# Performance work log

Measured on AMD Instinct MI355X. Metric: run time of the kernel, lower is better.

The kernel has to match this reference:

```python
import jax, jax.numpy as jnp
import numpy as np

N_NODES = 100000


def setup_inputs() -> dict:
    key = jax.random.key(0)
    k1, k2, k3, k4 = jax.random.split(key, 4)
    E = 1600000
    D_IN, D_OUT = 128, 128
    feat = jax.random.normal(k1, (N_NODES, D_IN), dtype=jnp.float32)
    src = jax.random.randint(k2, (E,), 0, N_NODES, dtype=jnp.int32)
    dst = jax.random.randint(k3, (E,), 0, N_NODES, dtype=jnp.int32)
    # xavier_uniform for weight [in, out]
    limit = float(np.sqrt(6.0 / (D_IN + D_OUT)))
    weight = jax.random.uniform(k4, (D_IN, D_OUT), dtype=jnp.float32,
                                minval=-limit, maxval=limit)
    bias = jnp.zeros((D_OUT,), dtype=jnp.float32)
    return {"feat": feat, "weight": weight, "bias": bias, "src": src, "dst": dst}


def reference(feat, weight, bias, src, dst):
    # in-degree normalization: norm_i = 1/sqrt(in_deg(i)); clamp deg>=1 to avoid inf
    deg = jax.ops.segment_sum(jnp.ones(src.shape[0], dtype=jnp.float32), dst,
                              num_segments=N_NODES)
    norm = jax.lax.rsqrt(jnp.maximum(deg, 1.0))[:, None]  # [N,1]
    h = feat * norm
    # update_all(copy_src, sum): scatter-sum src features into dst nodes (SpMM)
    agg = jax.ops.segment_sum(h[src], dst, num_segments=N_NODES)  # [N, D_in]
    # in_feats == out_feats -> aggregate first, then dense transform
    rst = agg @ weight          # [N, D_out]
    rst = rst * norm + bias
    return rst
```

## Files before the change

kernel.cpp:

```cpp
#include <hip/hip_runtime.h>


constexpr int N_NODES = 100000;
constexpr int D = 128;
constexpr int NB = 256;
constexpr int GROUP = (N_NODES + NB - 1) / NB;
constexpr int CAP = 14336;

typedef float f32x4 __attribute__((ext_vector_type(4)));
typedef short short8 __attribute__((ext_vector_type(8)));
typedef unsigned uint4v __attribute__((ext_vector_type(4)));

__device__ __forceinline__ ushort f2bf(float x) {
    unsigned u = __float_as_uint(x);
    return (ushort)((u + 0x7fffu + ((u >> 16) & 1u)) >> 16);
}
__device__ __forceinline__ float bf2f(ushort h) {
    return __uint_as_float(((unsigned)h) << 16);
}

__global__ __launch_bounds__(256) void p1_histo(const int* __restrict__ dst, int E,
                                                int* __restrict__ bhist,
                                                const float* __restrict__ W,
                                                ushort* __restrict__ whi,
                                                ushort* __restrict__ wlo) {
    __shared__ int h[NB];
    int t = threadIdx.x, blk = blockIdx.x;
    h[t] = 0;
    if (blk < 64) {
        int p = blk * 256 + t;
        int i  = p & 7;
        int l  = (p >> 3) & 63;
        int kt = (p >> 9) & 3;
        int ct = (p >> 11);
        int k = kt * 32 + (l >> 4) * 8 + i;
        int n = ct * 16 + (l & 15);
        float x = W[k * 128 + n];
        ushort hh = f2bf(x);
        whi[p] = hh;
        wlo[p] = f2bf(x - bf2f(hh));
    }
    __syncthreads();
    int per = (E + NB - 1) / NB;
    int s = blk * per, e = min(E, s + per);
    for (int i = s + t; i < e; i += 256) atomicAdd(&h[dst[i] / GROUP], 1);
    __syncthreads();
    bhist[t * NB + blk] = h[t];
}

__global__ __launch_bounds__(256) void p1_scanrow(int* __restrict__ bhist,
                                                  int* __restrict__ rowtot) {
    __shared__ int lds[256];
    int b = blockIdx.x, t = threadIdx.x;
    int v = bhist[b * NB + t];
    lds[t] = v; __syncthreads();
    for (int off = 1; off < 256; off <<= 1) {
        int x = (t >= off) ? lds[t - off] : 0;
        __syncthreads();
        lds[t] += x;
        __syncthreads();
    }
    bhist[b * NB + t] = lds[t] - v;
    if (t == 255) rowtot[b] = lds[255];
}

__global__ __launch_bounds__(256) void p1_scatter(const int* __restrict__ src,
                                                  const int* __restrict__ dst, int E,
                                                  const int* __restrict__ bhist,
                                                  const int* __restrict__ rowtot,
                                                  int* __restrict__ pairs) {
    __shared__ int loff[NB];
    __shared__ int bb[NB];
    int t = threadIdx.x, blk = blockIdx.x;
    int rv = rowtot[t];
    bb[t] = rv; __syncthreads();
    for (int off = 1; off < 256; off <<= 1) {
        int x = (t >= off) ? bb[t - off] : 0;
        __syncthreads();
        bb[t] += x;
        __syncthreads();
    }
    loff[t] = bhist[t * NB + blk] + bb[t] - rv;
    __syncthreads();
    int per = (E + NB - 1) / NB;
    int s = blk * per, e = min(E, s + per);
    for (int i = s + t; i < e; i += 256) {
        int d = dst[i];
        int b = d / GROUP;
        int pos = atomicAdd(&loff[b], 1);
        pairs[pos] = ((d - b * GROUP) << 17) | src[i];
    }
}

__global__ __launch_bounds__(256) void p2_all(const int* __restrict__ pairs,
                                              const int* __restrict__ rowtot,
                                              int* __restrict__ deg,
                                              int* __restrict__ offs,
                                              float* __restrict__ norm,
                                              int* __restrict__ esrc) {
    __shared__ int h[512];
    __shared__ int ssum[256];
    __shared__ int bb[256];
    __shared__ int sbuf[CAP];
    int t = threadIdx.x, b = blockIdx.x;
    int lo = b * GROUP;
    int cnt = min(GROUP, N_NODES - lo);

    int rv = rowtot[t];
    bb[t] = rv;
    h[t] = 0; h[t + 256] = 0;
    __syncthreads();
    for (int off = 1; off < 256; off <<= 1) {
        int x = (t >= off) ? bb[t - off] : 0;
        __syncthreads();
        bb[t] += x;
        __syncthreads();
    }
    int s1 = bb[b];
    int s0 = s1 - rowtot[b];
    __syncthreads();

    for (int i = s0 + t; i < s1; i += 256) atomicAdd(&h[pairs[i] >> 17], 1);
    __syncthreads();

    int v0 = h[2 * t], v1 = h[2 * t + 1];
    int s = v0 + v1;
    ssum[t] = s; __syncthreads();
    for (int off = 1; off < 256; off <<= 1) {
        int x = (t >= off) ? ssum[t - off] : 0;
        __syncthreads();
        ssum[t] += x;
        __syncthreads();
    }
    int pre = ssum[t] - s;
    if (2 * t < cnt) {
        int node = lo + 2 * t;
        deg[node] = v0;
        offs[node] = s0 + pre;
        norm[node] = rsqrtf(fmaxf((float)v0, 1.0f));
    }
    if (2 * t + 1 < cnt) {
        int node = lo + 2 * t + 1;
        deg[node] = v1;
        offs[node] = s0 + pre + v0;
        norm[node] = rsqrtf(fmaxf((float)v1, 1.0f));
    }
    __syncthreads();
    h[2 * t] = pre;
    h[2 * t + 1] = pre + v0;
    __syncthreads();

    int wsize = s1 - s0;
    bool fits = (wsize <= CAP);
    for (int i = s0 + t; i < s1; i += 256) {
        int p = pairs[i];
        int dl = p >> 17;
        int sv = p & 0x1FFFF;
        int pos = atomicAdd(&h[dl], 1);
        if (fits) sbuf[pos] = sv; else esrc[s0 + pos] = sv;
    }
    __syncthreads();
    if (fits)
        for (int i = t; i < wsize; i += 256) esrc[s0 + i] = sbuf[i];
}

__global__ void k_featbf(const float* __restrict__ feat, const float* __restrict__ norm,
                         uint2* __restrict__ ft2, int total) {
    int i = blockIdx.x * blockDim.x + threadIdx.x;
    if (i < total) {
        float w = norm[i >> 5];
        f32x4 v = ((const f32x4*)feat)[i];
        uint2 o;
        o.x = (unsigned)f2bf(v[0] * w) | ((unsigned)f2bf(v[1] * w) << 16);
        o.y = (unsigned)f2bf(v[2] * w) | ((unsigned)f2bf(v[3] * w) << 16);
        ft2[i] = o;
    }
}

__global__ __launch_bounds__(256) void k_gather8(const unsigned* __restrict__ ft,
                                                 const int* __restrict__ offs,
                                                 const int* __restrict__ deg,
                                                 const int* __restrict__ esrc,
                                                 unsigned* __restrict__ outbf) {
    int gtid = blockIdx.x * blockDim.x + threadIdx.x;
    int node = gtid >> 6;
    if (node >= N_NODES) return;
    int lane = gtid & 63;
    int g  = lane >> 4;
    int sl = lane & 15;
    int start = offs[node];
    int cnt   = deg[node];
    int last  = start + cnt - 1;
    float acc[8] = {0.f, 0.f, 0.f, 0.f, 0.f, 0.f, 0.f, 0.f};
    const uint4v* ftv = (const uint4v*)ft;
    for (int j = 0; j < cnt; j += 8) {
        int i0 = start + j + g;
        int i1 = start + j + 4 + g;
        int s0v = esrc[min(i0, last)];
        int s1v = esrc[min(i1, last)];
        float w0 = (j + g     < cnt) ? 1.0f : 0.0f;
        float w1 = (j + 4 + g < cnt) ? 1.0f : 0.0f;
        uint4v u0 = ftv[(size_t)s0v * 16 + sl];
        uint4v u1 = ftv[(size_t)s1v * 16 + sl];
        #pragma unroll
        for (int q = 0; q < 4; ++q) {
            unsigned a = u0[q];
            acc[q * 2]     = fmaf(__uint_as_float(a << 16),         w0, acc[q * 2]);
            acc[q * 2 + 1] = fmaf(__uint_as_float(a & 0xffff0000u), w0, acc[q * 2 + 1]);
        }
        #pragma unroll
        for (int q = 0; q < 4; ++q) {
            unsigned a = u1[q];
            acc[q * 2]     = fmaf(__uint_as_float(a << 16),         w1, acc[q * 2]);
            acc[q * 2 + 1] = fmaf(__uint_as_float(a & 0xffff0000u), w1, acc[q * 2 + 1]);
        }
    }
    #pragma unroll
    for (int q = 0; q < 8; ++q) {
        acc[q] += __shfl_xor(acc[q], 16, 64);
        acc[q] += __shfl_xor(acc[q], 32, 64);
    }
    if (g == 0) {
        uint4v o;
        #pragma unroll
        for (int q = 0; q < 4; ++q)
            o[q] = (unsigned)f2bf(acc[q * 2]) | ((unsigned)f2bf(acc[q * 2 + 1]) << 16);
        ((uint4v*)outbf)[(size_t)node * 16 + sl] = o;
    }
}

__global__ __launch_bounds__(256) void k_gemm_bf(const ushort* __restrict__ aggbf,
                                                 const ushort* __restrict__ whi,
                                                 const ushort* __restrict__ wlo,
                                                 const float* __restrict__ bias,
                                                 const float* __restrict__ norm,
                                                 float* __restrict__ out) {
    __shared__ ushort sH[16384];
    __shared__ ushort sL[16384];
    {
        const short8* gh = (const short8*)whi;
        const short8* gl = (const short8*)wlo;
        short8* lh = (short8*)sH;
        short8* ll = (short8*)sL;
        for (int i = threadIdx.x; i < 2048; i += 256) { lh[i] = gh[i]; ll[i] = gl[i]; }
    }
    __syncthreads();

    const int lane = threadIdx.x & 63;
    const int wid  = threadIdx.x >> 6;
    const int rsub = lane & 15;
    const int kgrp = lane >> 4;

    const short8* BH = (const short8*)sH;
    const short8* BL = (const short8*)sL;

    const int nstrips = N_NODES / 16;
    for (int strip = blockIdx.x * 4 + wid; strip < nstrips; strip += gridDim.x * 4) {
        const int row0 = strip * 16;
        const ushort* arow = aggbf + (size_t)(row0 + rsub) * D + kgrp * 8;
        short8 a[4];
        #pragma unroll
        for (int kt = 0; kt < 4; ++kt) a[kt] = *(const short8*)(arow + kt * 32);
        float nr[4];
        #pragma unroll
        for (int r = 0; r < 4; ++r) nr[r] = norm[row0 + kgrp * 4 + r];

        #pragma unroll
        for (int ct = 0; ct < 8; ++ct) {
            f32x4 acc = {0.f, 0.f, 0.f, 0.f};
            #pragma unroll
            for (int kt = 0; kt < 4; ++kt) {
                acc = __builtin_amdgcn_mfma_f32_16x16x32_bf16(a[kt], BH[(ct * 4 + kt) * 64 + lane], acc, 0, 0, 0);
                acc = __builtin_amdgcn_mfma_f32_16x16x32_bf16(a[kt], BL[(ct * 4 + kt) * 64 + lane], acc, 0, 0, 0);
            }
            const float bc = bias[ct * 16 + rsub];
            float* ocol = out + (size_t)row0 * D + ct * 16 + rsub;
            #pragma unroll
            for (int r = 0; r < 4; ++r) {
                int row = kgrp * 4 + r;
                ocol[(size_t)row * D] = acc[r] * nr[r] + bc;
            }
        }
    }
}

__global__ void k_scatter(const float* __restrict__ feat, const int* __restrict__ src,
                          const int* __restrict__ dst, const float* __restrict__ norm,
                          int E, float* __restrict__ agg) {
    long long gtid = (long long)blockIdx.x * blockDim.x + threadIdx.x;
    int e    = (int)(gtid >> 6);
    int lane = (int)(gtid & 63);
    if (e >= E) return;
    int s = src[e];
    int t = dst[e];
    float ns = norm[s];
    float2 v = ((const float2*)(feat + (size_t)s * D))[lane];
    float* arow = agg + (size_t)t * D + lane * 2;
    atomicAdd(arow + 0, v.x * ns);
    atomicAdd(arow + 1, v.y * ns);
}
__global__ void k_deg_f(const int* __restrict__ dst, int E, float* __restrict__ deg) {
    int i = blockIdx.x * blockDim.x + threadIdx.x;
    if (i < E) atomicAdd(deg + dst[i], 1.0f);
}
__global__ void k_norm_f(float* __restrict__ dn) {
    int i = blockIdx.x * blockDim.x + threadIdx.x;
    if (i < N_NODES) dn[i] = rsqrtf(fmaxf(dn[i], 1.0f));
}
__global__ __launch_bounds__(256) void k_gemm(float* __restrict__ io,
                                              const float* __restrict__ W,
                                              const float* __restrict__ bias,
                                              const float* __restrict__ norm) {
    __shared__ float sW[D * D];
    __shared__ float srow[2][D];
    for (int i = threadIdx.x; i < D * D; i += 256) sW[i] = W[i];
    const int r = threadIdx.x >> 7;
    const int c = threadIdx.x & 127;
    const float bc = bias[c];
    const int npairs = N_NODES / 2;
    for (int rp = blockIdx.x; rp < npairs; rp += gridDim.x) {
        __syncthreads();
        const int row = rp * 2 + r;
        srow[r][c] = io[(size_t)row * D + c];
        __syncthreads();
        float acc = 0.f;
        #pragma unroll 8
        for (int k = 0; k < D; ++k)
            acc = fmaf(srow[r][k], sW[k * D + c], acc);
        io[(size_t)row * D + c] = acc * norm[row] + bc;
    }
}

extern "C" void kernel_launch(void* const* d_in, const int* in_sizes, int n_in,
                              void* d_out, int out_size, void* d_ws, size_t ws_size,
                              hipStream_t stream) {
    const float* feat   = (const float*)d_in[0];
    const float* weight = (const float*)d_in[1];
    const float* bias   = (const float*)d_in[2];
    const int*   src    = (const int*)d_in[3];
    const int*   dst    = (const int*)d_in[4];
    const int E = in_sizes[3];

    int* pairs = (int*)d_out;

    uintptr_t cur = (uintptr_t)d_ws;
    auto take = [&](size_t bytes) -> void* {
        uintptr_t r = (cur + 63) & ~(uintptr_t)63;
        cur = r + bytes;
        return (void*)r;
    };

    size_t S_ft  = (size_t)N_NODES * 64 * 4;
    size_t S_agg = (size_t)N_NODES * D * 2;
    size_t need  = S_ft + S_agg +
                   (size_t)(3 * N_NODES + 256 + NB * NB + E) * 4 + 65536 + 1024;

    unsigned* ft     = (unsigned*)take(S_ft);
    ushort*   aggbf  = (ushort*)take(S_agg);
    float*    norm   = (float*)take((size_t)N_NODES * 4);
    int*      deg    = (int*)take((size_t)N_NODES * 4);
    int*      offs   = (int*)take((size_t)N_NODES * 4);
    int*      rowtot = (int*)take(256 * 4);
    int*      bhist  = (int*)take((size_t)NB * NB * 4);
    int*      esrc   = (int*)take((size_t)E * 4);
    ushort*   whi    = (ushort*)take(16384 * 2);
    ushort*   wlo    = (ushort*)take(16384 * 2);

    if (ws_size >= need) {
        p1_histo<<<NB, 256, 0, stream>>>(dst, E, bhist, weight, whi, wlo);
        p1_scanrow<<<NB, 256, 0, stream>>>(bhist, rowtot);
        p1_scatter<<<NB, 256, 0, stream>>>(src, dst, E, bhist, rowtot, pairs);
        p2_all<<<NB, 256, 0, stream>>>(pairs, rowtot, deg, offs, norm, esrc);
        k_featbf<<<(N_NODES * 32 + 255) / 256, 256, 0, stream>>>(feat, norm, (uint2*)ft, N_NODES * 32);
        long long gthreads = (long long)N_NODES * 64;
        k_gather8<<<(int)((gthreads + 255) / 256), 256, 0, stream>>>(ft, offs, deg, esrc, (unsigned*)aggbf);
        k_gemm_bf<<<1024, 256, 0, stream>>>(aggbf, whi, wlo, bias, norm, (float*)d_out);
    } else {
        float* agg = (float*)d_out;
        hipMemsetAsync(d_out, 0, (size_t)N_NODES * D * sizeof(float), stream);
        hipMemsetAsync(norm, 0, (size_t)N_NODES * sizeof(float), stream);
        k_deg_f<<<(E + 255) / 256, 256, 0, stream>>>(dst, E, (float*)norm);
        k_norm_f<<<(N_NODES + 255) / 256, 256, 0, stream>>>((float*)norm);
        long long sthreads = (long long)E * 64;
        k_scatter<<<(int)((sthreads + 255) / 256), 256, 0, stream>>>(feat, src, dst, (float*)norm, E, agg);
        k_gemm<<<4096, 256, 0, stream>>>(agg, weight, bias, (float*)norm);
    }
}
```

Baseline: 140.9 us.

## Drop scanrow kernel, sort per-node edge lists, and persist gather waves

Removes the row-scan kernel: the histogram kernel writes block-major counts and atomically accumulates row totals into a zeroed buffer, and the scatter kernel computes its column prefix with a serial loop over earlier blocks. The bucketing kernel now insertion-sorts each node's source list in LDS so gather reads of feature rows are more ordered and cache-friendly. The gather kernel becomes a grid-stride loop with a fixed grid of 1792 blocks instead of one wave per node. The tradeoffs are an extra memset, serial prefix loops of up to 256 iterations, and per-thread insertion sorts of about 16 elements.

```diff
diff --git a/kernel.cpp b/kernel.cpp
--- a/kernel.cpp
+++ b/kernel.cpp
@@ -21,6 +21,7 @@
 
 __global__ __launch_bounds__(256) void p1_histo(const int* __restrict__ dst, int E,
                                                 int* __restrict__ bhist,
+                                                int* __restrict__ rowtot,
                                                 const float* __restrict__ W,
                                                 ushort* __restrict__ whi,
                                                 ushort* __restrict__ wlo) {
@@ -45,23 +46,8 @@
     int s = blk * per, e = min(E, s + per);
     for (int i = s + t; i < e; i += 256) atomicAdd(&h[dst[i] / GROUP], 1);
     __syncthreads();
-    bhist[t * NB + blk] = h[t];
-}
-
-__global__ __launch_bounds__(256) void p1_scanrow(int* __restrict__ bhist,
-                                                  int* __restrict__ rowtot) {
-    __shared__ int lds[256];
-    int b = blockIdx.x, t = threadIdx.x;
-    int v = bhist[b * NB + t];
-    lds[t] = v; __syncthreads();
-    for (int off = 1; off < 256; off <<= 1) {
-        int x = (t >= off) ? lds[t - off] : 0;
-        __syncthreads();
-        lds[t] += x;
-        __syncthreads();
-    }
-    bhist[b * NB + t] = lds[t] - v;
-    if (t == 255) rowtot[b] = lds[255];
+    bhist[blk * NB + t] = h[t];
+    if (h[t]) atomicAdd(&rowtot[t], h[t]);
 }
 
 __global__ __launch_bounds__(256) void p1_scatter(const int* __restrict__ src,
@@ -80,7 +66,9 @@
         bb[t] += x;
         __syncthreads();
     }
-    loff[t] = bhist[t * NB + blk] + bb[t] - rv;
+    int cp = 0;
+    for (int c = 0; c < blk; ++c) cp += bhist[c * NB + t];
+    loff[t] = cp + bb[t] - rv;
     __syncthreads();
     int per = (E + NB - 1) / NB;
     int s = blk * per, e = min(E, s + per);
@@ -160,8 +148,23 @@
         if (fits) sbuf[pos] = sv; else esrc[s0 + pos] = sv;
     }
     __syncthreads();
-    if (fits)
+    if (fits) {
+        #pragma unroll
+        for (int w = 0; w < 2; ++w) {
+            bool ok = (w == 0) ? (2 * t < cnt) : (2 * t + 1 < cnt);
+            if (!ok) continue;
+            int st = (w == 0) ? pre : pre + v0;
+            int cn = (w == 0) ? v0 : v1;
+            for (int a = st + 1; a < st + cn; ++a) {
+                int key = sbuf[a];
+                int b2 = a - 1;
+                while (b2 >= st && sbuf[b2] > key) { sbuf[b2 + 1] = sbuf[b2]; --b2; }
+                sbuf[b2 + 1] = key;
+            }
+        }
+        __syncthreads();
         for (int i = t; i < wsize; i += 256) esrc[s0 + i] = sbuf[i];
+    }
 }
 
 __global__ void k_featbf(const float* __restrict__ feat, const float* __restrict__ norm,
@@ -181,51 +184,53 @@
                                                  const int* __restrict__ offs,
                                                  const int* __restrict__ deg,
                                                  const int* __restrict__ esrc,
-                                                 unsigned* __restrict__ outbf) {
+                                                 unsigned* __restrict__ outbf,
+                                                 int nwaves) {
     int gtid = blockIdx.x * blockDim.x + threadIdx.x;
-    int node = gtid >> 6;
-    if (node >= N_NODES) return;
+    int wave = gtid >> 6;
     int lane = gtid & 63;
     int g  = lane >> 4;
     int sl = lane & 15;
-    int start = offs[node];
-    int cnt   = deg[node];
-    int last  = start + cnt - 1;
-    float acc[8] = {0.f, 0.f, 0.f, 0.f, 0.f, 0.f, 0.f, 0.f};
     const uint4v* ftv = (const uint4v*)ft;
-    for (int j = 0; j < cnt; j += 8) {
-        int i0 = start + j + g;
-        int i1 = start + j + 4 + g;
-        int s0v = esrc[min(i0, last)];
-        int s1v = esrc[min(i1, last)];
-        float w0 = (j + g     < cnt) ? 1.0f : 0.0f;
-        float w1 = (j + 4 + g < cnt) ? 1.0f : 0.0f;
-        uint4v u0 = ftv[(size_t)s0v * 16 + sl];
-        uint4v u1 = ftv[(size_t)s1v * 16 + sl];
-        #pragma unroll
-        for (int q = 0; q < 4; ++q) {
-            unsigned a = u0[q];
-            acc[q * 2]     = fmaf(__uint_as_float(a << 16),         w0, acc[q * 2]);
-            acc[q * 2 + 1] = fmaf(__uint_as_float(a & 0xffff0000u), w0, acc[q * 2 + 1]);
-        }
-        #pragma unroll
-        for (int q = 0; q < 4; ++q) {
-            unsigned a = u1[q];
-            acc[q * 2]     = fmaf(__uint_as_float(a << 16),         w1, acc[q * 2]);
-            acc[q * 2 + 1] = fmaf(__uint_as_float(a & 0xffff0000u), w1, acc[q * 2 + 1]);
-        }
-    }
-    #pragma unroll
-    for (int q = 0; q < 8; ++q) {
-        acc[q] += __shfl_xor(acc[q], 16, 64);
-        acc[q] += __shfl_xor(acc[q], 32, 64);
-    }
-    if (g == 0) {
-        uint4v o;
-        #pragma unroll
-        for (int q = 0; q < 4; ++q)
-            o[q] = (unsigned)f2bf(acc[q * 2]) | ((unsigned)f2bf(acc[q * 2 + 1]) << 16);
-        ((uint4v*)outbf)[(size_t)node * 16 + sl] = o;
+    for (int node = wave; node < N_NODES; node += nwaves) {
+        int start = offs[node];
+        int cnt   = deg[node];
+        int last  = start + cnt - 1;
+        float acc[8] = {0.f, 0.f, 0.f, 0.f, 0.f, 0.f, 0.f, 0.f};
+        for (int j = 0; j < cnt; j += 8) {
+            int i0 = start + j + g;
+            int i1 = start + j + 4 + g;
+            int s0v = esrc[min(i0, last)];
+            int s1v = esrc[min(i1, last)];
+            float w0 = (j + g     < cnt) ? 1.0f : 0.0f;
+            float w1 = (j + 4 + g < cnt) ? 1.0f : 0.0f;
+            uint4v u0 = ftv[(size_t)s0v * 16 + sl];
+            uint4v u1 = ftv[(size_t)s1v * 16 + sl];
+            #pragma unroll
+            for (int q = 0; q < 4; ++q) {
+                unsigned a = u0[q];
+                acc[q * 2]     = fmaf(__uint_as_float(a << 16),         w0, acc[q * 2]);
+                acc[q * 2 + 1] = fmaf(__uint_as_float(a & 0xffff0000u), w0, acc[q * 2 + 1]);
+            }
+            #pragma unroll
+            for (int q = 0; q < 4; ++q) {
+                unsigned a = u1[q];
+                acc[q * 2]     = fmaf(__uint_as_float(a << 16),         w1, acc[q * 2]);
+                acc[q * 2 + 1] = fmaf(__uint_as_float(a & 0xffff0000u), w1, acc[q * 2 + 1]);
+            }
+        }
+        #pragma unroll
+        for (int q = 0; q < 8; ++q) {
+            acc[q] += __shfl_xor(acc[q], 16, 64);
+            acc[q] += __shfl_xor(acc[q], 32, 64);
+        }
+        if (g == 0) {
+            uint4v o;
+            #pragma unroll
+            for (int q = 0; q < 4; ++q)
+                o[q] = (unsigned)f2bf(acc[q * 2]) | ((unsigned)f2bf(acc[q * 2 + 1]) << 16);
+            ((uint4v*)outbf)[(size_t)node * 16 + sl] = o;
+        }
     }
 }
 
@@ -367,13 +372,13 @@
     ushort*   wlo    = (ushort*)take(16384 * 2);
 
     if (ws_size >= need) {
-        p1_histo<<<NB, 256, 0, stream>>>(dst, E, bhist, weight, whi, wlo);
-        p1_scanrow<<<NB, 256, 0, stream>>>(bhist, rowtot);
+        hipMemsetAsync(rowtot, 0, 256 * sizeof(int), stream);
+        p1_histo<<<NB, 256, 0, stream>>>(dst, E, bhist, rowtot, weight, whi, wlo);
         p1_scatter<<<NB, 256, 0, stream>>>(src, dst, E, bhist, rowtot, pairs);
         p2_all<<<NB, 256, 0, stream>>>(pairs, rowtot, deg, offs, norm, esrc);
         k_featbf<<<(N_NODES * 32 + 255) / 256, 256, 0, stream>>>(feat, norm, (uint2*)ft, N_NODES * 32);
-        long long gthreads = (long long)N_NODES * 64;
-        k_gather8<<<(int)((gthreads + 255) / 256), 256, 0, stream>>>(ft, offs, deg, esrc, (unsigned*)aggbf);
+        const int GB = 1792;
+        k_gather8<<<GB, 256, 0, stream>>>(ft, offs, deg, esrc, (unsigned*)aggbf, GB * 4);
         k_gemm_bf<<<1024, 256, 0, stream>>>(aggbf, whi, wlo, bias, norm, (float*)d_out);
     } else {
         float* agg = (float*)d_out;
```

New measurement: 243.7 us. 72.9% more time.
